# Optimization experiments

Measured on AMD Instinct MI355X. Metric: run time of the kernel, lower is better.

The kernel has to match this reference:

```python
import jax, jax.numpy as jnp
import numpy as np

DIM = 256
HEADS = 4
HEAD_DIM = DIM // HEADS          # 64
KEY_DIM = HEAD_DIM // 2          # 32 (attn_ratio=0.5)
HIDDEN = DIM + 2 * KEY_DIM * HEADS  # 512
B, H, W = 2, 64, 64
EPS = 1e-5


def _conv2d(x, w, groups=1, pad=0):
    return jax.lax.conv_general_dilated(
        x, w, window_strides=(1, 1), padding=[(pad, pad), (pad, pad)],
        dimension_numbers=('NCHW', 'OIHW', 'NCHW'), feature_group_count=groups)


def _bn(x, g, b, m, v):
    scale = g / jnp.sqrt(v + EPS)
    return x * scale[None, :, None, None] + (b - m * scale)[None, :, None, None]


def setup_inputs() -> dict:
    key = jax.random.key(0)
    ks = jax.random.split(key, 16)
    d = {
        'x': jax.random.normal(ks[0], (B, DIM, H, W), jnp.float32),
        'qkv_w': jax.random.normal(ks[1], (HIDDEN, DIM, 1, 1), jnp.float32) * 0.05,
        'qkv_g': jax.random.uniform(ks[2], (HIDDEN,), jnp.float32, 0.5, 1.5),
        'qkv_b': jax.random.normal(ks[3], (HIDDEN,), jnp.float32) * 0.1,
        'qkv_m': jax.random.normal(ks[4], (HIDDEN,), jnp.float32) * 0.1,
        'qkv_v': jax.random.uniform(ks[5], (HIDDEN,), jnp.float32, 0.5, 1.5),
        'proj_w': jax.random.normal(ks[6], (DIM, DIM, 1, 1), jnp.float32) * 0.05,
        'proj_g': jax.random.uniform(ks[7], (DIM,), jnp.float32, 0.5, 1.5),
        'proj_b': jax.random.normal(ks[8], (DIM,), jnp.float32) * 0.1,
        'proj_m': jax.random.normal(ks[9], (DIM,), jnp.float32) * 0.1,
        'proj_v': jax.random.uniform(ks[10], (DIM,), jnp.float32, 0.5, 1.5),
        'pe_w': jax.random.normal(ks[11], (DIM, 1, 3, 3), jnp.float32) * 0.1,
        'pe_g': jax.random.uniform(ks[12], (DIM,), jnp.float32, 0.5, 1.5),
        'pe_b': jax.random.normal(ks[13], (DIM,), jnp.float32) * 0.1,
        'pe_m': jax.random.normal(ks[14], (DIM,), jnp.float32) * 0.1,
        'pe_v': jax.random.uniform(ks[15], (DIM,), jnp.float32, 0.5, 1.5),
    }
    return d


def reference(x, qkv_w, qkv_g, qkv_b, qkv_m, qkv_v,
              proj_w, proj_g, proj_b, proj_m, proj_v,
              pe_w, pe_g, pe_b, pe_m, pe_v):
    b, c, h, w = x.shape
    n = h * w
    scale = KEY_DIM ** -0.5

    qkv = _bn(_conv2d(x, qkv_w), qkv_g, qkv_b, qkv_m, qkv_v)  # [b, hidden, h, w]
    qkv = qkv.reshape(b, HEADS, 2 * KEY_DIM + HEAD_DIM, n)
    q = qkv[:, :, :KEY_DIM]                       # [b, heads, key_dim, n]
    k = qkv[:, :, KEY_DIM:2 * KEY_DIM]            # [b, heads, key_dim, n]
    v = qkv[:, :, 2 * KEY_DIM:]                   # [b, heads, head_dim, n]

    # attn[b,h,i,j] = sum_d q[b,h,d,i] * k[b,h,d,j] * scale; softmax over j
    attn = jnp.einsum('bhdi,bhdj->bhij', q, k) * scale
    attn = jax.nn.softmax(attn, axis=-1)

    # y = v @ attn^T : out[b,h,d,i] = sum_j v[b,h,d,j] * attn[b,h,i,j]
    y = jnp.einsum('bhdj,bhij->bhdi', v, attn).reshape(b, c, h, w)

    pe = _bn(_conv2d(v.reshape(b, c, h, w), pe_w, groups=c, pad=1),
             pe_g, pe_b, pe_m, pe_v)
    y = y + pe
    return _bn(_conv2d(y, proj_w), proj_g, proj_b, proj_m, proj_v)
```

## Files before the change

kernel.cpp:

```cpp
#include <hip/hip_runtime.h>
#include <hip/hip_bf16.h>

#define NSP 4096
#define BEPS 1e-5f
#define JSPLIT 4
#define JCHUNK (NSP / JSPLIT)

using short8  = __attribute__((ext_vector_type(8))) short;
using half8   = __attribute__((ext_vector_type(8))) _Float16;
using f32x4   = __attribute__((ext_vector_type(4))) float;
using f32x16  = __attribute__((ext_vector_type(16))) float;

#define SCALE_LOG2E 0.2550348883f

__device__ __forceinline__ float b2f(unsigned short u) {
  return __uint_as_float(((unsigned)u) << 16);
}
__device__ __forceinline__ float b2f_lo(unsigned w) {
  return __uint_as_float(w << 16);
}
__device__ __forceinline__ float b2f_hi(unsigned w) {
  return __uint_as_float(w & 0xffff0000u);
}
__device__ __forceinline__ unsigned short f2b(float x) {
  unsigned u = __float_as_uint(x);
  u += 0x7fffu + ((u >> 16) & 1u);
  return (unsigned short)(u >> 16);
}
__device__ __forceinline__ unsigned pk_bf16(float a, float b) {
  return ((unsigned)f2b(b) << 16) | (unsigned)f2b(a);
}
__device__ __forceinline__ unsigned pk2u(float a, float b) {
  __hip_bfloat162 h = __float22bfloat162_rn(float2{a, b});
  unsigned r;
  __builtin_memcpy(&r, &h, sizeof(r));
  return r;
}
__device__ __forceinline__ unsigned short f2h(float x) {
  _Float16 h = (_Float16)x;
  unsigned short u;
  __builtin_memcpy(&u, &h, sizeof(u));
  return u;
}
__device__ __forceinline__ unsigned pk_h2(float a, float b) {
  return ((unsigned)f2h(b) << 16) | (unsigned)f2h(a);
}

__global__ __launch_bounds__(256) void cast_w_kernel(
    const float* __restrict__ qkv_w, const float* __restrict__ proj_w,
    unsigned short* __restrict__ wqb, unsigned short* __restrict__ wpb)
{
  const int i = blockIdx.x * 256 + threadIdx.x;
  if (i < 131072)       wqb[i] = f2h(qkv_w[i]);
  else                  wpb[i - 131072] = f2b(proj_w[i - 131072]);
}

__global__ __launch_bounds__(256) void transpose_x_kernel(
    const float* __restrict__ x, unsigned short* __restrict__ xT)
{
  const int n0 = blockIdx.x * 64, c0 = blockIdx.y * 64, b = blockIdx.z;
  __shared__ __align__(16) unsigned short tx[64][72];
  const int t = threadIdx.x;
  const int row = t >> 2;
  const int seg = t & 3;
  {
    const float* xp = x + ((size_t)(b * 256 + c0 + row)) * NSP + n0 + seg * 16;
    #pragma unroll
    for (int q4 = 0; q4 < 4; ++q4) {
      const float4 a = *reinterpret_cast<const float4*>(xp + q4 * 4);
      tx[seg * 16 + q4 * 4 + 0][row] = f2h(a.x);
      tx[seg * 16 + q4 * 4 + 1][row] = f2h(a.y);
      tx[seg * 16 + q4 * 4 + 2][row] = f2h(a.z);
      tx[seg * 16 + q4 * 4 + 3][row] = f2h(a.w);
    }
  }
  __syncthreads();
  const int nrow = t >> 2, ch = t & 3;
  unsigned short* op = xT + ((size_t)(b * NSP + n0 + nrow)) * 256 + c0 + ch * 16;
  *reinterpret_cast<float4*>(op)     = *reinterpret_cast<const float4*>(&tx[nrow][ch * 16]);
  *reinterpret_cast<float4*>(op + 8) = *reinterpret_cast<const float4*>(&tx[nrow][ch * 16 + 8]);
}

__global__ __launch_bounds__(256) void qkv_gemm_kernel(
    const unsigned short* __restrict__ xT, const unsigned short* __restrict__ wqb,
    const float* __restrict__ gg, const float* __restrict__ bb,
    const float* __restrict__ mm, const float* __restrict__ vv,
    unsigned short* __restrict__ qb, unsigned short* __restrict__ kb,
    unsigned short* __restrict__ vb)
{
  const int n0 = blockIdx.x * 128;
  const int cotile = blockIdx.y;
  const int b = blockIdx.z;
  const int co0 = cotile * 64;
  const int t = threadIdx.x;
  __shared__ __align__(16) unsigned short wt[64][136];
  __shared__ __align__(16) unsigned short xt[128][136];
  const int lane = t & 63, wave = t >> 6;
  const int m16 = lane & 15, quad = lane >> 4;

  f32x4 acc[8] = {};
  for (int kc = 0; kc < 2; ++kc) {
    if (kc) __syncthreads();
    {
      const unsigned short* wp = wqb + (size_t)(co0 + (t >> 2)) * 256 + kc * 128 + (t & 3) * 32;
      #pragma unroll
      for (int u = 0; u < 4; ++u)
        *reinterpret_cast<float4*>(&wt[t >> 2][(t & 3) * 32 + u * 8]) =
            *reinterpret_cast<const float4*>(wp + u * 8);
      const unsigned short* xp = xT + ((size_t)(b * NSP + n0 + (t >> 1))) * 256 + kc * 128 + (t & 1) * 64;
      #pragma unroll
      for (int u = 0; u < 8; ++u)
        *reinterpret_cast<float4*>(&xt[t >> 1][(t & 1) * 64 + u * 8]) =
            *reinterpret_cast<const float4*>(xp + u * 8);
    }
    __syncthreads();
    if ((cotile & 1) == 0) {
      #pragma unroll
      for (int ks = 0; ks < 4; ++ks) {
        const half8 af = *reinterpret_cast<const half8*>(&wt[wave * 16 + m16][ks * 32 + quad * 8]);
        #pragma unroll
        for (int nt = 0; nt < 8; ++nt) {
          const half8 bf = *reinterpret_cast<const half8*>(&xt[nt * 16 + m16][ks * 32 + quad * 8]);
          acc[nt] = __builtin_amdgcn_mfma_f32_16x16x32_f16(af, bf, acc[nt], 0, 0, 0);
        }
      }
    } else {
      #pragma unroll
      for (int ks = 0; ks < 4; ++ks) {
        const half8 bf = *reinterpret_cast<const half8*>(&wt[wave * 16 + m16][ks * 32 + quad * 8]);
        #pragma unroll
        for (int nt = 0; nt < 8; ++nt) {
          const half8 af = *reinterpret_cast<const half8*>(&xt[nt * 16 + m16][ks * 32 + quad * 8]);
          acc[nt] = __builtin_amdgcn_mfma_f32_16x16x32_f16(af, bf, acc[nt], 0, 0, 0);
        }
      }
    }
  }

  const int head = cotile >> 1;
  const int bh = b * 4 + head;
  if ((cotile & 1) == 0) {
    const int coh = wave * 16 + quad * 4;
    const bool isq = (coh < 32);
    const float fold = isq ? SCALE_LOG2E : 1.0f;
    float sc[4], bi[4];
    #pragma unroll
    for (int r = 0; r < 4; ++r) {
      const int c = co0 + coh + r;
      const float s0 = gg[c] * rsqrtf(vv[c] + BEPS);
      sc[r] = s0 * fold;
      bi[r] = (bb[c] - mm[c] * s0) * fold;
    }
    unsigned short* dst = isq ? qb : kb;
    const int d0 = coh & 31;
    #pragma unroll
    for (int nt = 0; nt < 8; ++nt) {
      const int i = n0 + nt * 16 + m16;
      uint2 pk2;
      pk2.x = pk_h2(acc[nt][0] * sc[0] + bi[0], acc[nt][1] * sc[1] + bi[1]);
      pk2.y = pk_h2(acc[nt][2] * sc[2] + bi[2], acc[nt][3] * sc[3] + bi[3]);
      *reinterpret_cast<uint2*>(dst + ((size_t)bh * NSP + i) * 32 + d0) = pk2;
    }
  } else {
    const int c = co0 + wave * 16 + m16;
    const float sc = gg[c] * rsqrtf(vv[c] + BEPS);
    const float bi = bb[c] - mm[c] * sc;
    const int d = wave * 16 + m16;
    #pragma unroll
    for (int nt = 0; nt < 8; ++nt) {
      const int j = n0 + nt * 16 + quad * 4;
      uint2 pk2;
      pk2.x = pk_bf16(acc[nt][0] * sc + bi, acc[nt][1] * sc + bi);
      pk2.y = pk_bf16(acc[nt][2] * sc + bi, acc[nt][3] * sc + bi);
      *reinterpret_cast<uint2*>(vb + ((size_t)(bh * 64 + d)) * NSP + j) = pk2;
    }
  }
}

__global__ __launch_bounds__(256, 4) void attn_kernel(
    const unsigned short* __restrict__ qb, const unsigned short* __restrict__ kb,
    const unsigned short* __restrict__ vb,
    unsigned short* __restrict__ Opart, float* __restrict__ lpart)
{
  const int i0    = blockIdx.x * 128;
  const int bh    = blockIdx.y;
  const int split = blockIdx.z;
  const int jbase = split * JCHUNK;
  const int t  = threadIdx.x;
  const int lane = t & 63, wave = t >> 6;
  const int l31 = lane & 31, hi = lane >> 5;

  __shared__ __align__(16) unsigned short qs[128][40];
  __shared__ __align__(16) unsigned short ks[64][40];
  __shared__ __align__(16) unsigned short vs[64][72];

  {
    const unsigned short* qp = qb + ((size_t)bh * NSP + i0) * 32;
    const int r = t >> 1, h = t & 1;
    *reinterpret_cast<float4*>(&qs[r][h * 16]) =
        *reinterpret_cast<const float4*>(qp + r * 32 + h * 16);
    *reinterpret_cast<float4*>(&qs[r][h * 16 + 8]) =
        *reinterpret_cast<const float4*>(qp + r * 32 + h * 16 + 8);
  }

  const int srow = t >> 2, schunk = t & 3;
  const unsigned short* kbase = kb + (size_t)bh * NSP * 32;
  const unsigned short* vbase = vb + (size_t)bh * 64 * NSP;

  float4 kreg, vreg0, vreg1;
  kreg  = *reinterpret_cast<const float4*>(kbase + (size_t)(jbase + srow) * 32 + schunk * 8);
  vreg0 = *reinterpret_cast<const float4*>(vbase + (size_t)srow * NSP + jbase + schunk * 16);
  vreg1 = *reinterpret_cast<const float4*>(vbase + (size_t)srow * NSP + jbase + schunk * 16 + 8);

  __syncthreads();
  half8 qfrag[2];
  qfrag[0] = *reinterpret_cast<const half8*>(&qs[wave * 32 + l31][hi * 8]);
  qfrag[1] = *reinterpret_cast<const half8*>(&qs[wave * 32 + l31][16 + hi * 8]);

  *reinterpret_cast<float4*>(&ks[srow][schunk * 8]) = kreg;
  *reinterpret_cast<float4*>(&vs[srow][schunk * 16]) = vreg0;
  *reinterpret_cast<float4*>(&vs[srow][schunk * 16 + 8]) = vreg1;
  __syncthreads();

  float rsum = 0.f;
  f32x16 oacc[2] = {};

  for (int jt0 = 0; jt0 < JCHUNK; jt0 += 64) {
    const bool more = (jt0 + 64) < JCHUNK;
    if (more) {
      const int jn = jbase + jt0 + 64;
      kreg  = *reinterpret_cast<const float4*>(kbase + (size_t)(jn + srow) * 32 + schunk * 8);
      vreg0 = *reinterpret_cast<const float4*>(vbase + (size_t)srow * NSP + jn + schunk * 16);
      vreg1 = *reinterpret_cast<const float4*>(vbase + (size_t)srow * NSP + jn + schunk * 16 + 8);
    }

    half8 kf[2][2];
    #pragma unroll
    for (int jt32 = 0; jt32 < 2; ++jt32) {
      kf[jt32][0] = *reinterpret_cast<const half8*>(&ks[jt32 * 32 + l31][hi * 8]);
      kf[jt32][1] = *reinterpret_cast<const half8*>(&ks[jt32 * 32 + l31][16 + hi * 8]);
    }

    #pragma unroll
    for (int jt32 = 0; jt32 < 2; ++jt32) {
      f32x16 sacc = {};
      sacc = __builtin_amdgcn_mfma_f32_32x32x16_f16(kf[jt32][0], qfrag[0], sacc, 0, 0, 0);
      sacc = __builtin_amdgcn_mfma_f32_32x32x16_f16(kf[jt32][1], qfrag[1], sacc, 0, 0, 0);

      unsigned pk[8];
      #pragma unroll
      for (int c = 0; c < 8; ++c) {
        const float p0 = __builtin_amdgcn_exp2f(sacc[2 * c]);
        const float p1 = __builtin_amdgcn_exp2f(sacc[2 * c + 1]);
        rsum += p0 + p1;
        pk[c] = pk2u(p0, p1);
      }

      #pragma unroll
      for (int kt = 0; kt < 2; ++kt) {
        const unsigned s_a0 = (unsigned)__shfl_xor((int)pk[4 * kt + 0], 32);
        const unsigned s_a1 = (unsigned)__shfl_xor((int)pk[4 * kt + 1], 32);
        const unsigned s_b0 = (unsigned)__shfl_xor((int)pk[4 * kt + 2], 32);
        const unsigned s_b1 = (unsigned)__shfl_xor((int)pk[4 * kt + 3], 32);
        uint4 aw;
        aw.x = hi ? s_b0 : pk[4 * kt + 0];
        aw.y = hi ? s_b1 : pk[4 * kt + 1];
        aw.z = hi ? pk[4 * kt + 2] : s_a0;
        aw.w = hi ? pk[4 * kt + 3] : s_a1;
        short8 af;
        __builtin_memcpy(&af, &aw, 16);
        #pragma unroll
        for (int dt = 0; dt < 2; ++dt) {
          const short8 vf = *reinterpret_cast<const short8*>(
              &vs[dt * 32 + l31][jt32 * 32 + kt * 16 + hi * 8]);
          oacc[dt] = __builtin_amdgcn_mfma_f32_32x32x16_bf16(af, vf, oacc[dt], 0, 0, 0);
        }
      }
    }

    if (more) {
      __syncthreads();
      *reinterpret_cast<float4*>(&ks[srow][schunk * 8]) = kreg;
      *reinterpret_cast<float4*>(&vs[srow][schunk * 16]) = vreg0;
      *reinterpret_cast<float4*>(&vs[srow][schunk * 16 + 8]) = vreg1;
      __syncthreads();
    }
  }

  {
    float rs = rsum;
    rs += __shfl_xor(rs, 32);
    if (hi == 0)
      lpart[((size_t)split * 8 + bh) * NSP + i0 + wave * 32 + l31] = rs;
  }

  #pragma unroll
  for (int dt = 0; dt < 2; ++dt) {
    const int d = dt * 32 + l31;
    #pragma unroll
    for (int R = 0; R < 4; ++R) {
      uint2 pk2;
      pk2.x = pk2u(oacc[dt][4 * R + 0], oacc[dt][4 * R + 1]);
      pk2.y = pk2u(oacc[dt][4 * R + 2], oacc[dt][4 * R + 3]);
      *reinterpret_cast<uint2*>(Opart +
          (((size_t)split * 8 + bh) * 64 + d) * NSP + i0 + wave * 32 + 8 * R + 4 * hi) = pk2;
    }
  }
}

__global__ __launch_bounds__(256) void fuse_kernel(
    const unsigned short* __restrict__ Opart, const float* __restrict__ lpart,
    const unsigned short* __restrict__ vb,
    const float* __restrict__ pw, const float* __restrict__ pg,
    const float* __restrict__ pb, const float* __restrict__ pm,
    const float* __restrict__ pv,
    unsigned short* __restrict__ yT)
{
  const int py = blockIdx.x;
  const int bh = blockIdx.y;
  const int b = bh >> 2, h = bh & 3;
  const int t = threadIdx.x;
  const int d = t >> 2, seg = t & 3;
  __shared__ float lsum[64];
  __shared__ __align__(16) unsigned short yt[64][72];

  if (t < 64) {
    float ls = 0.f;
    #pragma unroll
    for (int s = 0; s < JSPLIT; ++s)
      ls += lpart[((size_t)s * 8 + bh) * NSP + py * 64 + t];
    lsum[t] = ls;
  }
  __syncthreads();

  const int c = h * 64 + d;
  const int i0 = py * 64 + seg * 16;
  float os[16] = {};
  #pragma unroll
  for (int s = 0; s < JSPLIT; ++s) {
    const uint4* op = reinterpret_cast<const uint4*>(
        Opart + (((size_t)s * 8 + bh) * 64 + d) * NSP + i0);
    const uint4 a = op[0], e = op[1];
    os[0]  += b2f_lo(a.x); os[1]  += b2f_hi(a.x);
    os[2]  += b2f_lo(a.y); os[3]  += b2f_hi(a.y);
    os[4]  += b2f_lo(a.z); os[5]  += b2f_hi(a.z);
    os[6]  += b2f_lo(a.w); os[7]  += b2f_hi(a.w);
    os[8]  += b2f_lo(e.x); os[9]  += b2f_hi(e.x);
    os[10] += b2f_lo(e.y); os[11] += b2f_hi(e.y);
    os[12] += b2f_lo(e.z); os[13] += b2f_hi(e.z);
    os[14] += b2f_lo(e.w); os[15] += b2f_hi(e.w);
  }

  float w9[9];
  #pragma unroll
  for (int i = 0; i < 9; ++i) w9[i] = pw[c * 9 + i];
  const float sc = pg[c] * rsqrtf(pv[c] + BEPS);
  const float bi = pb[c] - pm[c] * sc;
  const unsigned short* vrow = vb + ((size_t)(bh * 64 + d)) * NSP;

  float conv[16] = {};
  #pragma unroll
  for (int dy = -1; dy <= 1; ++dy) {
    const int yy = py + dy;
    if (yy < 0 || yy > 63) continue;
    const unsigned short* vr = vrow + yy * 64 + seg * 16;
    float vals[18];
    const uint4 m0 = *reinterpret_cast<const uint4*>(vr);
    const uint4 m1 = *reinterpret_cast<const uint4*>(vr + 8);
    vals[1]  = b2f_lo(m0.x); vals[2]  = b2f_hi(m0.x);
    vals[3]  = b2f_lo(m0.y); vals[4]  = b2f_hi(m0.y);
    vals[5]  = b2f_lo(m0.z); vals[6]  = b2f_hi(m0.z);
    vals[7]  = b2f_lo(m0.w); vals[8]  = b2f_hi(m0.w);
    vals[9]  = b2f_lo(m1.x); vals[10] = b2f_hi(m1.x);
    vals[11] = b2f_lo(m1.y); vals[12] = b2f_hi(m1.y);
    vals[13] = b2f_lo(m1.z); vals[14] = b2f_hi(m1.z);
    vals[15] = b2f_lo(m1.w); vals[16] = b2f_hi(m1.w);
    vals[0]  = (seg > 0) ? b2f_hi(*reinterpret_cast<const unsigned*>(vr - 2)) : 0.f;
    vals[17] = (seg < 3) ? b2f_lo(*reinterpret_cast<const unsigned*>(vr + 16)) : 0.f;
    const float wr0 = w9[(dy + 1) * 3 + 0], wr1 = w9[(dy + 1) * 3 + 1], wr2 = w9[(dy + 1) * 3 + 2];
    #pragma unroll
    for (int u = 0; u < 16; ++u)
      conv[u] += vals[u] * wr0 + vals[u + 1] * wr1 + vals[u + 2] * wr2;
  }

  #pragma unroll
  for (int u = 0; u < 16; ++u) {
    const float yv = os[u] / lsum[seg * 16 + u] + conv[u] * sc + bi;
    yt[seg * 16 + u][d] = f2b(yv);
  }
  __syncthreads();

  const int prow = t >> 2, ch = t & 3;
  unsigned short* op = yT + ((size_t)(b * NSP + py * 64 + prow)) * 256 + h * 64 + ch * 16;
  *reinterpret_cast<float4*>(op)     = *reinterpret_cast<const float4*>(&yt[prow][ch * 16]);
  *reinterpret_cast<float4*>(op + 8) = *reinterpret_cast<const float4*>(&yt[prow][ch * 16 + 8]);
}

__global__ __launch_bounds__(256) void proj_gemm_kernel(
    const unsigned short* __restrict__ yT, const unsigned short* __restrict__ wpb,
    const float* __restrict__ gg, const float* __restrict__ bb,
    const float* __restrict__ mm, const float* __restrict__ vv,
    float* __restrict__ out)
{
  const int n0 = blockIdx.x * 128;
  const int co0 = blockIdx.y * 64;
  const int b = blockIdx.z;
  const int t = threadIdx.x;
  __shared__ __align__(16) unsigned short wt[64][136];
  __shared__ __align__(16) unsigned short yt[128][136];
  const int lane = t & 63, wave = t >> 6;
  const int m16 = lane & 15, quad = lane >> 4;

  f32x4 acc[8] = {};
  for (int kc = 0; kc < 2; ++kc) {
    if (kc) __syncthreads();
    {
      const unsigned short* wp = wpb + (size_t)(co0 + (t >> 2)) * 256 + kc * 128 + (t & 3) * 32;
      #pragma unroll
      for (int u = 0; u < 4; ++u)
        *reinterpret_cast<float4*>(&wt[t >> 2][(t & 3) * 32 + u * 8]) =
            *reinterpret_cast<const float4*>(wp + u * 8);
      const unsigned short* yp = yT + ((size_t)(b * NSP + n0 + (t >> 1))) * 256 + kc * 128 + (t & 1) * 64;
      #pragma unroll
      for (int u = 0; u < 8; ++u)
        *reinterpret_cast<float4*>(&yt[t >> 1][(t & 1) * 64 + u * 8]) =
            *reinterpret_cast<const float4*>(yp + u * 8);
    }
    __syncthreads();
    #pragma unroll
    for (int ks = 0; ks < 4; ++ks) {
      const short8 bf = *reinterpret_cast<const short8*>(&wt[wave * 16 + m16][ks * 32 + quad * 8]);
      #pragma unroll
      for (int nt = 0; nt < 8; ++nt) {
        const short8 af = *reinterpret_cast<const short8*>(&yt[nt * 16 + m16][ks * 32 + quad * 8]);
        acc[nt] = __builtin_amdgcn_mfma_f32_16x16x32_bf16(af, bf, acc[nt], 0, 0, 0);
      }
    }
  }

  const int c = co0 + wave * 16 + m16;
  const float sc = gg[c] * rsqrtf(vv[c] + BEPS);
  const float bi = bb[c] - mm[c] * sc;
  #pragma unroll
  for (int nt = 0; nt < 8; ++nt) {
    const int n = n0 + nt * 16 + quad * 4;
    float4 ov;
    ov.x = acc[nt][0] * sc + bi; ov.y = acc[nt][1] * sc + bi;
    ov.z = acc[nt][2] * sc + bi; ov.w = acc[nt][3] * sc + bi;
    *reinterpret_cast<float4*>(out + ((size_t)(b * 256 + c)) * NSP + n) = ov;
  }
}

extern "C" void kernel_launch(void* const* d_in, const int* in_sizes, int n_in,
                              void* d_out, int out_size, void* d_ws, size_t ws_size,
                              hipStream_t stream)
{
  const float* x      = (const float*)d_in[0];
  const float* qkv_w  = (const float*)d_in[1];
  const float* qkv_g  = (const float*)d_in[2];
  const float* qkv_b  = (const float*)d_in[3];
  const float* qkv_m  = (const float*)d_in[4];
  const float* qkv_v  = (const float*)d_in[5];
  const float* proj_w = (const float*)d_in[6];
  const float* proj_g = (const float*)d_in[7];
  const float* proj_b = (const float*)d_in[8];
  const float* proj_m = (const float*)d_in[9];
  const float* proj_v = (const float*)d_in[10];
  const float* pe_w   = (const float*)d_in[11];
  const float* pe_g   = (const float*)d_in[12];
  const float* pe_b   = (const float*)d_in[13];
  const float* pe_m   = (const float*)d_in[14];
  const float* pe_v   = (const float*)d_in[15];
  float* out = (float*)d_out;

  unsigned short* qb = (unsigned short*)d_ws;
  unsigned short* kb = qb + (size_t)8 * NSP * 32;
  unsigned short* vb = kb + (size_t)8 * NSP * 32;
  unsigned short* Opart = vb + (size_t)8 * 64 * NSP;
  float* lpart = (float*)(Opart + (size_t)JSPLIT * 8 * 64 * NSP);
  unsigned short* xT = (unsigned short*)(lpart + (size_t)JSPLIT * 8 * NSP);
  unsigned short* yT = xT + (size_t)2 * NSP * 256;
  unsigned short* wqb = yT + (size_t)2 * NSP * 256;
  unsigned short* wpb = wqb + (size_t)512 * 256;

  cast_w_kernel<<<dim3(768), 256, 0, stream>>>(qkv_w, proj_w, wqb, wpb);
  transpose_x_kernel<<<dim3(64, 4, 2), 256, 0, stream>>>(x, xT);
  qkv_gemm_kernel<<<dim3(32, 8, 2), 256, 0, stream>>>(xT, wqb, qkv_g, qkv_b, qkv_m, qkv_v,
                                                      qb, kb, vb);
  attn_kernel<<<dim3(32, 8, JSPLIT), 256, 0, stream>>>(qb, kb, vb, Opart, lpart);
  fuse_kernel<<<dim3(64, 8), 256, 0, stream>>>(Opart, lpart, vb,
                                               pe_w, pe_g, pe_b, pe_m, pe_v, yT);
  proj_gemm_kernel<<<dim3(32, 4, 2), 256, 0, stream>>>(yT, wpb, proj_g, proj_b, proj_m, proj_v,
                                                       out);
}
```

Before: 158.6 us.

## Raise attention occupancy, split keys eightfold, and halve proj GEMM tile

The attention kernel now aliases the Q and K shared-memory buffers (with an added barrier) and raises launch bounds to 8 blocks per CU, so more waves fit per CU. When the workspace is large enough it uses 8 key splits instead of 4, which doubles the attention grid and the partial buffers the fuse kernel has to reduce. The fuse kernel multiplies by a precomputed reciprocal of the softmax sum instead of dividing, and the projection GEMM uses 64-column tiles for twice as many blocks. The risks are register spilling under the tighter launch bound and extra partial-output traffic with 8 splits.

```diff
diff --git a/kernel.cpp b/kernel.cpp
--- a/kernel.cpp
+++ b/kernel.cpp
@@ -3,8 +3,6 @@
 
 #define NSP 4096
 #define BEPS 1e-5f
-#define JSPLIT 4
-#define JCHUNK (NSP / JSPLIT)
 
 using short8  = __attribute__((ext_vector_type(8))) short;
 using half8   = __attribute__((ext_vector_type(8))) _Float16;
@@ -177,22 +175,25 @@
   }
 }
 
-__global__ __launch_bounds__(256, 4) void attn_kernel(
+template<int JS>
+__global__ __launch_bounds__(256, 8) void attn_kernel(
     const unsigned short* __restrict__ qb, const unsigned short* __restrict__ kb,
     const unsigned short* __restrict__ vb,
     unsigned short* __restrict__ Opart, float* __restrict__ lpart)
 {
+  constexpr int JCH = NSP / JS;
   const int i0    = blockIdx.x * 128;
   const int bh    = blockIdx.y;
   const int split = blockIdx.z;
-  const int jbase = split * JCHUNK;
+  const int jbase = split * JCH;
   const int t  = threadIdx.x;
   const int lane = t & 63, wave = t >> 6;
   const int l31 = lane & 31, hi = lane >> 5;
 
-  __shared__ __align__(16) unsigned short qs[128][40];
-  __shared__ __align__(16) unsigned short ks[64][40];
-  __shared__ __align__(16) unsigned short vs[64][72];
+  __shared__ __align__(16) unsigned short smem[7168];
+  unsigned short (*qs)[40] = (unsigned short(*)[40])smem;
+  unsigned short (*ks)[40] = (unsigned short(*)[40])smem;
+  unsigned short (*vs)[72] = (unsigned short(*)[72])(smem + 2560);
 
   {
     const unsigned short* qp = qb + ((size_t)bh * NSP + i0) * 32;
@@ -216,6 +217,7 @@
   half8 qfrag[2];
   qfrag[0] = *reinterpret_cast<const half8*>(&qs[wave * 32 + l31][hi * 8]);
   qfrag[1] = *reinterpret_cast<const half8*>(&qs[wave * 32 + l31][16 + hi * 8]);
+  __syncthreads();
 
   *reinterpret_cast<float4*>(&ks[srow][schunk * 8]) = kreg;
   *reinterpret_cast<float4*>(&vs[srow][schunk * 16]) = vreg0;
@@ -225,8 +227,8 @@
   float rsum = 0.f;
   f32x16 oacc[2] = {};
 
-  for (int jt0 = 0; jt0 < JCHUNK; jt0 += 64) {
-    const bool more = (jt0 + 64) < JCHUNK;
+  for (int jt0 = 0; jt0 < JCH; jt0 += 64) {
+    const bool more = (jt0 + 64) < JCH;
     if (more) {
       const int jn = jbase + jt0 + 64;
       kreg  = *reinterpret_cast<const float4*>(kbase + (size_t)(jn + srow) * 32 + schunk * 8);
@@ -308,6 +310,7 @@
   }
 }
 
+template<int JS>
 __global__ __launch_bounds__(256) void fuse_kernel(
     const unsigned short* __restrict__ Opart, const float* __restrict__ lpart,
     const unsigned short* __restrict__ vb,
@@ -327,9 +330,9 @@
   if (t < 64) {
     float ls = 0.f;
     #pragma unroll
-    for (int s = 0; s < JSPLIT; ++s)
+    for (int s = 0; s < JS; ++s)
       ls += lpart[((size_t)s * 8 + bh) * NSP + py * 64 + t];
-    lsum[t] = ls;
+    lsum[t] = 1.0f / ls;
   }
   __syncthreads();
 
@@ -337,7 +340,7 @@
   const int i0 = py * 64 + seg * 16;
   float os[16] = {};
   #pragma unroll
-  for (int s = 0; s < JSPLIT; ++s) {
+  for (int s = 0; s < JS; ++s) {
     const uint4* op = reinterpret_cast<const uint4*>(
         Opart + (((size_t)s * 8 + bh) * 64 + d) * NSP + i0);
     const uint4 a = op[0], e = op[1];
@@ -385,7 +388,7 @@
 
   #pragma unroll
   for (int u = 0; u < 16; ++u) {
-    const float yv = os[u] / lsum[seg * 16 + u] + conv[u] * sc + bi;
+    const float yv = os[u] * lsum[seg * 16 + u] + conv[u] * sc + bi;
     yt[seg * 16 + u][d] = f2b(yv);
   }
   __syncthreads();
@@ -402,16 +405,16 @@
     const float* __restrict__ mm, const float* __restrict__ vv,
     float* __restrict__ out)
 {
-  const int n0 = blockIdx.x * 128;
+  const int n0 = blockIdx.x * 64;
   const int co0 = blockIdx.y * 64;
   const int b = blockIdx.z;
   const int t = threadIdx.x;
   __shared__ __align__(16) unsigned short wt[64][136];
-  __shared__ __align__(16) unsigned short yt[128][136];
+  __shared__ __align__(16) unsigned short yt[64][136];
   const int lane = t & 63, wave = t >> 6;
   const int m16 = lane & 15, quad = lane >> 4;
 
-  f32x4 acc[8] = {};
+  f32x4 acc[4] = {};
   for (int kc = 0; kc < 2; ++kc) {
     if (kc) __syncthreads();
     {
@@ -420,10 +423,10 @@
       for (int u = 0; u < 4; ++u)
         *reinterpret_cast<float4*>(&wt[t >> 2][(t & 3) * 32 + u * 8]) =
             *reinterpret_cast<const float4*>(wp + u * 8);
-      const unsigned short* yp = yT + ((size_t)(b * NSP + n0 + (t >> 1))) * 256 + kc * 128 + (t & 1) * 64;
-      #pragma unroll
-      for (int u = 0; u < 8; ++u)
-        *reinterpret_cast<float4*>(&yt[t >> 1][(t & 1) * 64 + u * 8]) =
+      const unsigned short* yp = yT + ((size_t)(b * NSP + n0 + (t >> 2))) * 256 + kc * 128 + (t & 3) * 32;
+      #pragma unroll
+      for (int u = 0; u < 4; ++u)
+        *reinterpret_cast<float4*>(&yt[t >> 2][(t & 3) * 32 + u * 8]) =
             *reinterpret_cast<const float4*>(yp + u * 8);
     }
     __syncthreads();
@@ -431,7 +434,7 @@
     for (int ks = 0; ks < 4; ++ks) {
       const short8 bf = *reinterpret_cast<const short8*>(&wt[wave * 16 + m16][ks * 32 + quad * 8]);
       #pragma unroll
-      for (int nt = 0; nt < 8; ++nt) {
+      for (int nt = 0; nt < 4; ++nt) {
         const short8 af = *reinterpret_cast<const short8*>(&yt[nt * 16 + m16][ks * 32 + quad * 8]);
         acc[nt] = __builtin_amdgcn_mfma_f32_16x16x32_bf16(af, bf, acc[nt], 0, 0, 0);
       }
@@ -442,7 +445,7 @@
   const float sc = gg[c] * rsqrtf(vv[c] + BEPS);
   const float bi = bb[c] - mm[c] * sc;
   #pragma unroll
-  for (int nt = 0; nt < 8; ++nt) {
+  for (int nt = 0; nt < 4; ++nt) {
     const int n = n0 + nt * 16 + quad * 4;
     float4 ov;
     ov.x = acc[nt][0] * sc + bi; ov.y = acc[nt][1] * sc + bi;
@@ -473,12 +476,15 @@
   const float* pe_v   = (const float*)d_in[15];
   float* out = (float*)d_out;
 
+  const size_t need8 = 51773440u;
+  const int JS = (ws_size >= need8) ? 8 : 4;
+
   unsigned short* qb = (unsigned short*)d_ws;
   unsigned short* kb = qb + (size_t)8 * NSP * 32;
   unsigned short* vb = kb + (size_t)8 * NSP * 32;
   unsigned short* Opart = vb + (size_t)8 * 64 * NSP;
-  float* lpart = (float*)(Opart + (size_t)JSPLIT * 8 * 64 * NSP);
-  unsigned short* xT = (unsigned short*)(lpart + (size_t)JSPLIT * 8 * NSP);
+  float* lpart = (float*)(Opart + (size_t)JS * 8 * 64 * NSP);
+  unsigned short* xT = (unsigned short*)(lpart + (size_t)JS * 8 * NSP);
   unsigned short* yT = xT + (size_t)2 * NSP * 256;
   unsigned short* wqb = yT + (size_t)2 * NSP * 256;
   unsigned short* wpb = wqb + (size_t)512 * 256;
@@ -487,9 +493,15 @@
   transpose_x_kernel<<<dim3(64, 4, 2), 256, 0, stream>>>(x, xT);
   qkv_gemm_kernel<<<dim3(32, 8, 2), 256, 0, stream>>>(xT, wqb, qkv_g, qkv_b, qkv_m, qkv_v,
                                                       qb, kb, vb);
-  attn_kernel<<<dim3(32, 8, JSPLIT), 256, 0, stream>>>(qb, kb, vb, Opart, lpart);
-  fuse_kernel<<<dim3(64, 8), 256, 0, stream>>>(Opart, lpart, vb,
-                                               pe_w, pe_g, pe_b, pe_m, pe_v, yT);
-  proj_gemm_kernel<<<dim3(32, 4, 2), 256, 0, stream>>>(yT, wpb, proj_g, proj_b, proj_m, proj_v,
+  if (JS == 8) {
+    attn_kernel<8><<<dim3(32, 8, 8), 256, 0, stream>>>(qb, kb, vb, Opart, lpart);
+    fuse_kernel<8><<<dim3(64, 8), 256, 0, stream>>>(Opart, lpart, vb,
+                                                    pe_w, pe_g, pe_b, pe_m, pe_v, yT);
+  } else {
+    attn_kernel<4><<<dim3(32, 8, 4), 256, 0, stream>>>(qb, kb, vb, Opart, lpart);
+    fuse_kernel<4><<<dim3(64, 8), 256, 0, stream>>>(Opart, lpart, vb,
+                                                    pe_w, pe_g, pe_b, pe_m, pe_v, yT);
+  }
+  proj_gemm_kernel<<<dim3(64, 4, 2), 256, 0, stream>>>(yT, wpb, proj_g, proj_b, proj_m, proj_v,
                                                        out);
 }
```

Result: slower. 448.4 us (+182.8%).
